# Optimization experiments

Hardware: AMD Instinct MI355X
Metric: run time of the kernel (lower is better)

The kernel has to match this reference:

```python
import jax, jax.numpy as jnp
import numpy as np

N = 100000
IN_CH = 128
OUT_CH = 40
K = 2
E = 3200000


def setup_inputs() -> dict:
    key = jax.random.key(0)
    k1, k2, k3, k4 = jax.random.split(key, 4)
    x = jax.random.normal(k1, (N, IN_CH), dtype=jnp.float32)
    edge_index = jax.random.randint(k2, (2, E), 0, N, dtype=jnp.int64)
    # Linear params (PyG Linear: glorot-style init approximated)
    scale = 1.0 / np.sqrt(IN_CH)
    W = jax.random.uniform(k3, (IN_CH, OUT_CH), dtype=jnp.float32, minval=-scale, maxval=scale)
    b = jax.random.uniform(k4, (OUT_CH,), dtype=jnp.float32, minval=-scale, maxval=scale)
    return {"x": x, "edge_index": edge_index, "W": W, "b": b}


def reference(x, edge_index, W, b):
    n = x.shape[0]
    row, col = edge_index[0], edge_index[1]  # source -> target
    # gcn_norm: add self loops, symmetric normalization
    loop = jnp.arange(n, dtype=row.dtype)
    row = jnp.concatenate([row, loop])
    col = jnp.concatenate([col, loop])
    ones = jnp.ones(row.shape[0], dtype=x.dtype)
    deg = jax.ops.segment_sum(ones, col, num_segments=n)  # in-degree incl. self-loop
    deg_inv_sqrt = jnp.where(deg > 0, jax.lax.rsqrt(deg), 0.0)
    norm = deg_inv_sqrt[row] * deg_inv_sqrt[col]  # [E+N]
    h = x
    for _ in range(K):
        # sparse SpMM: out[col] += norm * h[row]
        h = jax.ops.segment_sum(norm[:, None] * h[row], col, num_segments=n)
    logits = h @ W + b
    return jax.nn.log_softmax(logits, axis=-1)
```

## Files before the change

### kernel.cpp

```cpp
#include <hip/hip_runtime.h>
#include <hip/hip_fp16.h>
#include <math.h>

#define NN 100000
#define ICH 128
#define OCH 40
#define NE 3200000
#define BSH 8
#define BNODES 256
#define BMASK 255
#define NB 391
#define CAP 9216
#define TILE 4096
#define NBIN ((NE + TILE - 1) / TILE)
#define YSTRIDE 40
#define YU2 (YSTRIDE / 8)
#define XWBLK 1563

typedef __attribute__((ext_vector_type(2))) float floatx2;
typedef __attribute__((ext_vector_type(4))) float floatx4;
typedef __attribute__((ext_vector_type(8))) short bf16x8;

__device__ __forceinline__ unsigned int pk_bf16(float a, float b) {
    unsigned int r;
    asm("v_cvt_pk_bf16_f32 %0, %1, %2" : "=v"(r) : "v"(a), "v"(b));
    return r;
}

__device__ __forceinline__ void acc_fp8x8(const uint2 u, float* acc) {
    floatx2 p0 = __builtin_amdgcn_cvt_pk_f32_fp8((int)u.x, false);
    floatx2 p1 = __builtin_amdgcn_cvt_pk_f32_fp8((int)u.x, true);
    floatx2 p2 = __builtin_amdgcn_cvt_pk_f32_fp8((int)u.y, false);
    floatx2 p3 = __builtin_amdgcn_cvt_pk_f32_fp8((int)u.y, true);
    acc[0] += p0.x; acc[1] += p0.y; acc[2] += p1.x; acc[3] += p1.y;
    acc[4] += p2.x; acc[5] += p2.y; acc[6] += p3.x; acc[7] += p3.y;
}

__device__ __forceinline__ uint2 pack_fp8x8(const float* v) {
    int lo = 0, hi = 0;
    lo = __builtin_amdgcn_cvt_pk_fp8_f32(v[0], v[1], lo, false);
    lo = __builtin_amdgcn_cvt_pk_fp8_f32(v[2], v[3], lo, true);
    hi = __builtin_amdgcn_cvt_pk_fp8_f32(v[4], v[5], hi, false);
    hi = __builtin_amdgcn_cvt_pk_fp8_f32(v[6], v[7], hi, true);
    return make_uint2((unsigned int)lo, (unsigned int)hi);
}

__device__ __forceinline__ void row_gather(const int* __restrict__ csr, int kb, int ke, int q,
                                           const uint2* __restrict__ base, float* acc) {
    int k = kb;
    if (k + 8 <= ke) {
        int s[8];
        uint2 v[8];
#pragma unroll
        for (int j = 0; j < 8; ++j) s[j] = csr[k + j];
#pragma unroll
        for (int j = 0; j < 8; ++j) v[j] = base[(size_t)s[j] * YU2 + q];
        k += 8;
        for (; k + 8 <= ke; k += 8) {
            int s2[8];
            uint2 w[8];
#pragma unroll
            for (int j = 0; j < 8; ++j) s2[j] = csr[k + j];
#pragma unroll
            for (int j = 0; j < 8; ++j) w[j] = base[(size_t)s2[j] * YU2 + q];
#pragma unroll
            for (int j = 0; j < 8; ++j) acc_fp8x8(v[j], acc);
#pragma unroll
            for (int j = 0; j < 8; ++j) v[j] = w[j];
        }
#pragma unroll
        for (int j = 0; j < 8; ++j) acc_fp8x8(v[j], acc);
    }
    for (; k < ke; ++k) acc_fp8x8(base[(size_t)csr[k] * YU2 + q], acc);
}

__global__ __launch_bounds__(512) void k_bin(const int* __restrict__ ei, int* __restrict__ bcursor,
                                             unsigned int* __restrict__ packed,
                                             const float* __restrict__ W, unsigned int* __restrict__ wbf) {
    __shared__ unsigned int entries[TILE];
    __shared__ unsigned short bid[TILE];
    __shared__ int hist[512], base[512], gbase[512], cur[512];
    int t = threadIdx.x;
    int tile0 = blockIdx.x * TILE;
    int tcnt = min(TILE, NE - tile0);
    hist[t] = 0;
    __syncthreads();
    int src[8], dst[8];
#pragma unroll
    for (int i = 0; i < 8; ++i) {
        int l = t + i * 512;
        if (l < tcnt) {
            int e = tile0 + l;
            src[i] = ei[e];
            dst[i] = ei[NE + e];
            atomicAdd(&hist[dst[i] >> BSH], 1);
        } else dst[i] = -1;
    }
    __syncthreads();
    int own = hist[t];
    base[t] = own;
    __syncthreads();
    for (int off = 1; off < 512; off <<= 1) {
        int v = (t >= off) ? base[t - off] : 0;
        __syncthreads();
        base[t] += v;
        __syncthreads();
    }
    int excl = base[t] - own;
    __syncthreads();
    base[t] = excl;
    cur[t] = excl;
    if (t < NB && own > 0) gbase[t] = atomicAdd(&bcursor[t], own);
    __syncthreads();
#pragma unroll
    for (int i = 0; i < 8; ++i) {
        if (dst[i] >= 0) {
            int bb = dst[i] >> BSH;
            int pos = atomicAdd(&cur[bb], 1);
            entries[pos] = ((unsigned int)(dst[i] & BMASK) << 17) | (unsigned int)src[i];
            bid[pos] = (unsigned short)bb;
        }
    }
    __syncthreads();
    for (int l = t; l < tcnt; l += 512) {
        int bb = bid[l];
        packed[(size_t)bb * CAP + gbase[bb] + (l - base[bb])] = entries[l];
    }
    if (blockIdx.x == 0) {
        for (int e = t; e < 1536; e += 512) {
            int hs = e / 768;
            int rem = e - hs * 768;
            int ss = rem / 192;
            int rem2 = rem - ss * 192;
            int n = rem2 >> 6;
            int lane = rem2 & 63;
            int kbase = ss * 32 + (lane >> 4) * 8;
            int col = n * 16 + (lane & 15);
            unsigned int u4[4];
#pragma unroll
            for (int p = 0; p < 4; ++p) {
                float f0 = (col < OCH) ? W[(size_t)(kbase + 2 * p) * OCH + col] : 0.f;
                float f1 = (col < OCH) ? W[(size_t)(kbase + 2 * p + 1) * OCH + col] : 0.f;
                unsigned int h = pk_bf16(f0, f1);
                if (hs == 0) {
                    u4[p] = h;
                } else {
                    float l0 = f0 - __uint_as_float(h << 16);
                    float l1 = f1 - __uint_as_float(h & 0xFFFF0000u);
                    u4[p] = pk_bf16(l0, l1);
                }
            }
            ((uint4*)wbf)[e] = make_uint4(u4[0], u4[1], u4[2], u4[3]);
        }
    }
}

__global__ __launch_bounds__(512) void k_csr(const int* __restrict__ bcursor,
                                             const unsigned int* __restrict__ packed,
                                             int* __restrict__ rowptr, float* __restrict__ dis,
                                             int* __restrict__ csr) {
    __shared__ int hist[BNODES], cur[BNODES], ps[BNODES], sred[512];
    int b = blockIdx.x;
    int t = threadIdx.x;
    int part = 0;
    for (int j = t; j < b; j += 512) part += bcursor[j];
    sred[t] = part;
    if (t < BNODES) hist[t] = 0;
    __syncthreads();
    for (int off = 256; off > 0; off >>= 1) {
        if (t < off) sred[t] += sred[t + off];
        __syncthreads();
    }
    int cbase = sred[0];
    int cnt = bcursor[b];
    int node0 = b << BSH;
    int nn = min(BNODES, NN - node0);
    const unsigned int* pk = packed + (size_t)b * CAP;
    for (int l = t; l < cnt; l += 512) atomicAdd(&hist[pk[l] >> 17], 1);
    __syncthreads();
    if (t < BNODES) ps[t] = hist[t];
    __syncthreads();
    for (int off = 1; off < BNODES; off <<= 1) {
        int u = (t >= off && t < BNODES) ? ps[t - off] : 0;
        __syncthreads();
        if (t < BNODES) ps[t] += u;
        __syncthreads();
    }
    if (t < BNODES) {
        int excl = ps[t] - hist[t];
        cur[t] = excl;
        if (t < nn) {
            rowptr[node0 + t] = cbase + excl;
            dis[node0 + t] = rsqrtf((float)hist[t] + 1.0f);
        }
    }
    if (b == 0 && t == 0) rowptr[NN] = NE;
    __syncthreads();
    for (int l = t; l < cnt; l += 512) {
        unsigned int e = pk[l];
        int pos = atomicAdd(&cur[e >> 17], 1);
        csr[cbase + pos] = (int)(e & 0x1FFFF);
    }
}

__global__ __launch_bounds__(128) void k_xw(const float* __restrict__ x, const unsigned int* __restrict__ wbf,
                                            const float* __restrict__ dis, unsigned char* __restrict__ y0) {
    int t = threadIdx.x;
    int wid = t >> 6, lane = t & 63;
    const bf16x8* wf = (const bf16x8*)wbf;
    bf16x8 whi[4][3], wlo[4][3];
#pragma unroll
    for (int s = 0; s < 4; ++s)
#pragma unroll
        for (int n = 0; n < 3; ++n) {
            whi[s][n] = wf[(s * 3 + n) * 64 + lane];
            wlo[s][n] = wf[768 + (s * 3 + n) * 64 + lane];
        }
    int rbase = blockIdx.x * 64 + wid * 32;
#pragma unroll
    for (int tt = 0; tt < 2; ++tt) {
        int r0 = rbase + tt * 16;
        int rowa = r0 + (lane & 15);
        int rowc = min(rowa, NN - 1);
        int kb = (lane >> 4) * 8;
        const float4* xp = (const float4*)(x + (size_t)rowc * ICH + kb);
        float4 xa[4][2];
#pragma unroll
        for (int s = 0; s < 4; ++s) {
            xa[s][0] = xp[s * 8];
            xa[s][1] = xp[s * 8 + 1];
        }
        floatx4 acc[3] = {{0.f, 0.f, 0.f, 0.f}, {0.f, 0.f, 0.f, 0.f}, {0.f, 0.f, 0.f, 0.f}};
#pragma unroll
        for (int s = 0; s < 4; ++s) {
            float f[8] = {xa[s][0].x, xa[s][0].y, xa[s][0].z, xa[s][0].w,
                          xa[s][1].x, xa[s][1].y, xa[s][1].z, xa[s][1].w};
            union { unsigned int u[4]; bf16x8 v; } ah, al;
#pragma unroll
            for (int p = 0; p < 4; ++p) {
                unsigned int h = pk_bf16(f[2 * p], f[2 * p + 1]);
                ah.u[p] = h;
                float l0 = f[2 * p] - __uint_as_float(h << 16);
                float l1 = f[2 * p + 1] - __uint_as_float(h & 0xFFFF0000u);
                al.u[p] = pk_bf16(l0, l1);
            }
#pragma unroll
            for (int n = 0; n < 3; ++n) {
                acc[n] = __builtin_amdgcn_mfma_f32_16x16x32_bf16(ah.v, whi[s][n], acc[n], 0, 0, 0);
                acc[n] = __builtin_amdgcn_mfma_f32_16x16x32_bf16(al.v, whi[s][n], acc[n], 0, 0, 0);
                acc[n] = __builtin_amdgcn_mfma_f32_16x16x32_bf16(ah.v, wlo[s][n], acc[n], 0, 0, 0);
            }
        }
        int rc0 = r0 + (lane >> 4) * 4;
        float dd[4];
#pragma unroll
        for (int r = 0; r < 4; ++r) dd[r] = (rc0 + r < NN) ? dis[rc0 + r] : 0.f;
#pragma unroll
        for (int n = 0; n < 3; ++n) {
            int col = n * 16 + (lane & 15);
            if (col < OCH) {
#pragma unroll
                for (int r = 0; r < 4; ++r) {
                    int row = rc0 + r;
                    if (row < NN) {
                        float val = acc[n][r] * dd[r];
                        int p8 = __builtin_amdgcn_cvt_pk_fp8_f32(val, val, 0, false);
                        y0[(size_t)row * YSTRIDE + col] = (unsigned char)(p8 & 0xFF);
                    }
                }
            }
        }
    }
}

__global__ __launch_bounds__(256) void k_hop1(const int* __restrict__ rowptr, const int* __restrict__ csr,
                                              const float* __restrict__ dis, const unsigned char* __restrict__ y0,
                                              unsigned char* __restrict__ y1) {
    int g = blockIdx.x * 256 + threadIdx.x;
    if (g >= NN * 5) return;
    int i = g / 5, q = g - 5 * i;
    const uint2* base = (const uint2*)y0;
    float acc[8];
#pragma unroll
    for (int j = 0; j < 8; ++j) acc[j] = 0.f;
    acc_fp8x8(base[(size_t)i * YU2 + q], acc);
    row_gather(csr, rowptr[i], rowptr[i + 1], q, base, acc);
    float d = dis[i], d2 = d * d;
#pragma unroll
    for (int j = 0; j < 8; ++j) acc[j] *= d2;
    ((uint2*)y1)[(size_t)i * YU2 + q] = pack_fp8x8(acc);
}

__global__ __launch_bounds__(320) void k_hop2f(const int* __restrict__ rowptr, const int* __restrict__ csr,
                                               const float* __restrict__ dis, const unsigned char* __restrict__ y1,
                                               const float* __restrict__ b, float* __restrict__ out) {
    __shared__ float red[64][5];
    int tid = threadIdx.x;
    int lg = tid / 5;
    int q = tid - 5 * lg;
    int g = blockIdx.x * 64 + lg;
    bool active = (g < NN);
    float l[8];
    if (active) {
        const uint2* base = (const uint2*)y1;
        float acc[8];
#pragma unroll
        for (int j = 0; j < 8; ++j) acc[j] = 0.f;
        acc_fp8x8(base[(size_t)g * YU2 + q], acc);
        row_gather(csr, rowptr[g], rowptr[g + 1], q, base, acc);
        float d = dis[g];
#pragma unroll
        for (int j = 0; j < 8; ++j) l[j] = d * acc[j] + b[8 * q + j];
    } else {
#pragma unroll
        for (int j = 0; j < 8; ++j) l[j] = -1e30f;
    }
    float m8 = l[0];
#pragma unroll
    for (int j = 1; j < 8; ++j) m8 = fmaxf(m8, l[j]);
    red[lg][q] = m8;
    __syncthreads();
    float gm = red[lg][0];
#pragma unroll
    for (int j = 1; j < 5; ++j) gm = fmaxf(gm, red[lg][j]);
    __syncthreads();
    float s8 = 0.f;
#pragma unroll
    for (int j = 0; j < 8; ++j) s8 += __expf(l[j] - gm);
    red[lg][q] = s8;
    __syncthreads();
    float gs = red[lg][0];
#pragma unroll
    for (int j = 1; j < 5; ++j) gs += red[lg][j];
    float ls = __logf(gs) + gm;
    if (active) {
        floatx4* orow = (floatx4*)(out + (size_t)g * OCH + 8 * q);
        floatx4 o0 = {l[0] - ls, l[1] - ls, l[2] - ls, l[3] - ls};
        floatx4 o1 = {l[4] - ls, l[5] - ls, l[6] - ls, l[7] - ls};
        __builtin_nontemporal_store(o0, orow);
        __builtin_nontemporal_store(o1, orow + 1);
    }
}

extern "C" void kernel_launch(void* const* d_in, const int* in_sizes, int n_in,
                              void* d_out, int out_size, void* d_ws, size_t ws_size,
                              hipStream_t stream) {
    const float* x  = (const float*)d_in[0];
    const int*   ei = (const int*)d_in[1];
    const float* W  = (const float*)d_in[2];
    const float* b  = (const float*)d_in[3];
    float* out = (float*)d_out;

    char* ws = (char*)d_ws;
    int*           bcursor = (int*)(ws + 0);
    int*           rowptr  = (int*)(ws + 4096);
    float*         dis     = (float*)(ws + 409600);
    unsigned int*  wbf     = (unsigned int*)(ws + 811008);
    unsigned int*  packed  = (unsigned int*)(ws + 843776);
    unsigned char* y0      = (unsigned char*)(ws + 843776);
    unsigned char* y1      = (unsigned char*)(ws + 4849664);
    int*           csr     = (int*)(ws + 15261696);

    hipMemsetAsync(bcursor, 0, NB * sizeof(int), stream);
    k_bin<<<NBIN, 512, 0, stream>>>(ei, bcursor, packed, W, wbf);
    k_csr<<<NB, 512, 0, stream>>>(bcursor, packed, rowptr, dis, csr);
    k_xw<<<XWBLK, 128, 0, stream>>>(x, wbf, dis, y0);
    k_hop1<<<(NN * 5 + 255) / 256, 256, 0, stream>>>(rowptr, csr, dis, y0, y1);
    k_hop2f<<<(NN + 63) / 64, 320, 0, stream>>>(rowptr, csr, dis, y1, b, out);
}
```

Measured before the change: 238.2 us.

## Replace two-pass binned CSR build with global-atomic degree count and scatter

Replaces the tile-binning plus per-bucket CSR construction with a plain counting sort: global atomic degree histogram, block sums, per-block prefix scan into rowptr and a cursor array, then an atomic scatter of sources into csr. This drops the packed intermediate buffer and the shared-memory binning passes. In exchange it issues millions of global atomics on random addresses and writes csr in scattered order, which also makes the within-row edge order nondeterministic and loses locality in the scatter writes.

```diff
diff --git a/kernel.cpp b/kernel.cpp
--- a/kernel.cpp
+++ b/kernel.cpp
@@ -8,11 +8,7 @@
 #define NE 3200000
 #define BSH 8
 #define BNODES 256
-#define BMASK 255
 #define NB 391
-#define CAP 9216
-#define TILE 4096
-#define NBIN ((NE + TILE - 1) / TILE)
 #define YSTRIDE 40
 #define YU2 (YSTRIDE / 8)
 #define XWBLK 1563
@@ -74,60 +70,19 @@
     for (; k < ke; ++k) acc_fp8x8(base[(size_t)csr[k] * YU2 + q], acc);
 }
 
-__global__ __launch_bounds__(512) void k_bin(const int* __restrict__ ei, int* __restrict__ bcursor,
-                                             unsigned int* __restrict__ packed,
+__global__ __launch_bounds__(256) void k_deg(const int* __restrict__ ei, int* __restrict__ deg,
                                              const float* __restrict__ W, unsigned int* __restrict__ wbf) {
-    __shared__ unsigned int entries[TILE];
-    __shared__ unsigned short bid[TILE];
-    __shared__ int hist[512], base[512], gbase[512], cur[512];
-    int t = threadIdx.x;
-    int tile0 = blockIdx.x * TILE;
-    int tcnt = min(TILE, NE - tile0);
-    hist[t] = 0;
-    __syncthreads();
-    int src[8], dst[8];
-#pragma unroll
-    for (int i = 0; i < 8; ++i) {
-        int l = t + i * 512;
-        if (l < tcnt) {
-            int e = tile0 + l;
-            src[i] = ei[e];
-            dst[i] = ei[NE + e];
-            atomicAdd(&hist[dst[i] >> BSH], 1);
-        } else dst[i] = -1;
-    }
-    __syncthreads();
-    int own = hist[t];
-    base[t] = own;
-    __syncthreads();
-    for (int off = 1; off < 512; off <<= 1) {
-        int v = (t >= off) ? base[t - off] : 0;
-        __syncthreads();
-        base[t] += v;
-        __syncthreads();
-    }
-    int excl = base[t] - own;
-    __syncthreads();
-    base[t] = excl;
-    cur[t] = excl;
-    if (t < NB && own > 0) gbase[t] = atomicAdd(&bcursor[t], own);
-    __syncthreads();
-#pragma unroll
-    for (int i = 0; i < 8; ++i) {
-        if (dst[i] >= 0) {
-            int bb = dst[i] >> BSH;
-            int pos = atomicAdd(&cur[bb], 1);
-            entries[pos] = ((unsigned int)(dst[i] & BMASK) << 17) | (unsigned int)src[i];
-            bid[pos] = (unsigned short)bb;
-        }
-    }
-    __syncthreads();
-    for (int l = t; l < tcnt; l += 512) {
-        int bb = bid[l];
-        packed[(size_t)bb * CAP + gbase[bb] + (l - base[bb])] = entries[l];
+    int e0 = (blockIdx.x * 256 + threadIdx.x) * 4;
+    if (e0 < NE) {
+        int4 d = *(const int4*)(ei + NE + e0);
+        atomicAdd(&deg[d.x], 1);
+        atomicAdd(&deg[d.y], 1);
+        atomicAdd(&deg[d.z], 1);
+        atomicAdd(&deg[d.w], 1);
     }
     if (blockIdx.x == 0) {
-        for (int e = t; e < 1536; e += 512) {
+        int t = threadIdx.x;
+        for (int e = t; e < 1536; e += 256) {
             int hs = e / 768;
             int rem = e - hs * 768;
             int ss = rem / 192;
@@ -155,52 +110,66 @@
     }
 }
 
-__global__ __launch_bounds__(512) void k_csr(const int* __restrict__ bcursor,
-                                             const unsigned int* __restrict__ packed,
-                                             int* __restrict__ rowptr, float* __restrict__ dis,
-                                             int* __restrict__ csr) {
-    __shared__ int hist[BNODES], cur[BNODES], ps[BNODES], sred[512];
-    int b = blockIdx.x;
-    int t = threadIdx.x;
+__global__ __launch_bounds__(256) void k_bsum(const int* __restrict__ deg, int* __restrict__ bsum) {
+    __shared__ int s[256];
+    int b = blockIdx.x, t = threadIdx.x;
+    int node = (b << BSH) + t;
+    s[t] = (node < NN) ? deg[node] : 0;
+    __syncthreads();
+    for (int off = 128; off > 0; off >>= 1) {
+        if (t < off) s[t] += s[t + off];
+        __syncthreads();
+    }
+    if (t == 0) bsum[b] = s[0];
+}
+
+__global__ __launch_bounds__(256) void k_rowptr(const int* __restrict__ deg, const int* __restrict__ bsum,
+                                                int* __restrict__ rowptr, int* __restrict__ cur,
+                                                float* __restrict__ dis) {
+    __shared__ int sred[256], ps[BNODES];
+    int b = blockIdx.x, t = threadIdx.x;
     int part = 0;
-    for (int j = t; j < b; j += 512) part += bcursor[j];
+    for (int j = t; j < b; j += 256) part += bsum[j];
     sred[t] = part;
-    if (t < BNODES) hist[t] = 0;
-    __syncthreads();
-    for (int off = 256; off > 0; off >>= 1) {
+    __syncthreads();
+    for (int off = 128; off > 0; off >>= 1) {
         if (t < off) sred[t] += sred[t + off];
         __syncthreads();
     }
     int cbase = sred[0];
-    int cnt = bcursor[b];
-    int node0 = b << BSH;
-    int nn = min(BNODES, NN - node0);
-    const unsigned int* pk = packed + (size_t)b * CAP;
-    for (int l = t; l < cnt; l += 512) atomicAdd(&hist[pk[l] >> 17], 1);
-    __syncthreads();
-    if (t < BNODES) ps[t] = hist[t];
+    int node = (b << BSH) + t;
+    int d = (node < NN) ? deg[node] : 0;
+    ps[t] = d;
     __syncthreads();
     for (int off = 1; off < BNODES; off <<= 1) {
-        int u = (t >= off && t < BNODES) ? ps[t - off] : 0;
+        int u = (t >= off) ? ps[t - off] : 0;
         __syncthreads();
-        if (t < BNODES) ps[t] += u;
+        ps[t] += u;
         __syncthreads();
     }
-    if (t < BNODES) {
-        int excl = ps[t] - hist[t];
-        cur[t] = excl;
-        if (t < nn) {
-            rowptr[node0 + t] = cbase + excl;
-            dis[node0 + t] = rsqrtf((float)hist[t] + 1.0f);
-        }
+    if (node < NN) {
+        int excl = cbase + ps[t] - d;
+        rowptr[node] = excl;
+        cur[node] = excl;
+        dis[node] = rsqrtf((float)d + 1.0f);
     }
     if (b == 0 && t == 0) rowptr[NN] = NE;
-    __syncthreads();
-    for (int l = t; l < cnt; l += 512) {
-        unsigned int e = pk[l];
-        int pos = atomicAdd(&cur[e >> 17], 1);
-        csr[cbase + pos] = (int)(e & 0x1FFFF);
-    }
+}
+
+__global__ __launch_bounds__(256) void k_scat(const int* __restrict__ ei, int* __restrict__ cur,
+                                              int* __restrict__ csr) {
+    int e0 = (blockIdx.x * 256 + threadIdx.x) * 4;
+    if (e0 >= NE) return;
+    int4 s = *(const int4*)(ei + e0);
+    int4 d = *(const int4*)(ei + NE + e0);
+    int p0 = atomicAdd(&cur[d.x], 1);
+    int p1 = atomicAdd(&cur[d.y], 1);
+    int p2 = atomicAdd(&cur[d.z], 1);
+    int p3 = atomicAdd(&cur[d.w], 1);
+    csr[p0] = s.x;
+    csr[p1] = s.y;
+    csr[p2] = s.z;
+    csr[p3] = s.w;
 }
 
 __global__ __launch_bounds__(128) void k_xw(const float* __restrict__ x, const unsigned int* __restrict__ wbf,
@@ -352,18 +321,21 @@
     float* out = (float*)d_out;
 
     char* ws = (char*)d_ws;
-    int*           bcursor = (int*)(ws + 0);
-    int*           rowptr  = (int*)(ws + 4096);
-    float*         dis     = (float*)(ws + 409600);
-    unsigned int*  wbf     = (unsigned int*)(ws + 811008);
-    unsigned int*  packed  = (unsigned int*)(ws + 843776);
-    unsigned char* y0      = (unsigned char*)(ws + 843776);
-    unsigned char* y1      = (unsigned char*)(ws + 4849664);
-    int*           csr     = (int*)(ws + 15261696);
-
-    hipMemsetAsync(bcursor, 0, NB * sizeof(int), stream);
-    k_bin<<<NBIN, 512, 0, stream>>>(ei, bcursor, packed, W, wbf);
-    k_csr<<<NB, 512, 0, stream>>>(bcursor, packed, rowptr, dis, csr);
+    int*           rowptr = (int*)(ws + 0);
+    float*         dis    = (float*)(ws + 409600);
+    int*           deg    = (int*)(ws + 819200);
+    int*           cur    = (int*)(ws + 1228800);
+    int*           bsum   = (int*)(ws + 1630208);
+    unsigned int*  wbf    = (unsigned int*)(ws + 1638400);
+    unsigned char* y0     = (unsigned char*)(ws + 1703936);
+    unsigned char* y1     = (unsigned char*)(ws + 5709824);
+    int*           csr    = (int*)(ws + 9715712);
+
+    hipMemsetAsync(deg, 0, NN * sizeof(int), stream);
+    k_deg<<<(NE / 4 + 255) / 256, 256, 0, stream>>>(ei, deg, W, wbf);
+    k_bsum<<<NB, 256, 0, stream>>>(deg, bsum);
+    k_rowptr<<<NB, 256, 0, stream>>>(deg, bsum, rowptr, cur, dis);
+    k_scat<<<(NE / 4 + 255) / 256, 256, 0, stream>>>(ei, cur, csr);
     k_xw<<<XWBLK, 128, 0, stream>>>(x, wbf, dis, y0);
     k_hop1<<<(NN * 5 + 255) / 256, 256, 0, stream>>>(rowptr, csr, dis, y0, y1);
     k_hop2f<<<(NN + 63) / 64, 320, 0, stream>>>(rowptr, csr, dis, y1, b, out);
```

Result: slower. 597.1 us (+150.7%).

## Wave-align hop node groups, share CSR indices and reduce softmax via shuffles

Applied to the files above, without the earlier changes.

Both hop kernels now map each node's five lanes to a fixed group inside one wave, 12 nodes per wave and 48 per 256-thread block; the last 4 lanes of each wave sit idle. Within a group, four lanes each load two CSR neighbor indices as a uint2 and broadcast them with __shfl, replacing eight scalar index loads per lane. In the final hop, the log-softmax max and sum reductions move from shared memory with __syncthreads to in-wave shuffles. The aim is fewer redundant index loads and no block barriers, at the cost of about 6% idle lanes and uint2 CSR loads that may be only 4-byte aligned.

```diff
diff --git a/kernel.cpp b/kernel.cpp
--- a/kernel.cpp
+++ b/kernel.cpp
@@ -16,6 +16,8 @@
 #define YSTRIDE 40
 #define YU2 (YSTRIDE / 8)
 #define XWBLK 1563
+#define HOPNPB 48
+#define HOPGRID ((NN + HOPNPB - 1) / HOPNPB)
 
 typedef __attribute__((ext_vector_type(2))) float floatx2;
 typedef __attribute__((ext_vector_type(4))) float floatx4;
@@ -45,24 +47,30 @@
     return make_uint2((unsigned int)lo, (unsigned int)hi);
 }
 
-__device__ __forceinline__ void row_gather(const int* __restrict__ csr, int kb, int ke, int q,
-                                           const uint2* __restrict__ base, float* acc) {
+__device__ __forceinline__ void grp_csr8(const int* __restrict__ csr, int k, int q, int base, int* s) {
+    uint2 c = make_uint2(0u, 0u);
+    if (q < 4) c = *(const uint2*)(csr + k + 2 * q);
+#pragma unroll
+    for (int j = 0; j < 8; ++j)
+        s[j] = __shfl((j & 1) ? (int)c.y : (int)c.x, base + (j >> 1), 64);
+}
+
+__device__ __forceinline__ void row_gather(const int* __restrict__ csr, int kb, int ke, int q, int base,
+                                           const uint2* __restrict__ yb, float* acc) {
     int k = kb;
     if (k + 8 <= ke) {
         int s[8];
         uint2 v[8];
-#pragma unroll
-        for (int j = 0; j < 8; ++j) s[j] = csr[k + j];
-#pragma unroll
-        for (int j = 0; j < 8; ++j) v[j] = base[(size_t)s[j] * YU2 + q];
+        grp_csr8(csr, k, q, base, s);
+#pragma unroll
+        for (int j = 0; j < 8; ++j) v[j] = yb[(size_t)s[j] * YU2 + q];
         k += 8;
         for (; k + 8 <= ke; k += 8) {
             int s2[8];
             uint2 w[8];
-#pragma unroll
-            for (int j = 0; j < 8; ++j) s2[j] = csr[k + j];
-#pragma unroll
-            for (int j = 0; j < 8; ++j) w[j] = base[(size_t)s2[j] * YU2 + q];
+            grp_csr8(csr, k, q, base, s2);
+#pragma unroll
+            for (int j = 0; j < 8; ++j) w[j] = yb[(size_t)s2[j] * YU2 + q];
 #pragma unroll
             for (int j = 0; j < 8; ++j) acc_fp8x8(v[j], acc);
 #pragma unroll
@@ -71,7 +79,7 @@
 #pragma unroll
         for (int j = 0; j < 8; ++j) acc_fp8x8(v[j], acc);
     }
-    for (; k < ke; ++k) acc_fp8x8(base[(size_t)csr[k] * YU2 + q], acc);
+    for (; k < ke; ++k) acc_fp8x8(yb[(size_t)csr[k] * YU2 + q], acc);
 }
 
 __global__ __launch_bounds__(512) void k_bin(const int* __restrict__ ei, int* __restrict__ bcursor,
@@ -276,70 +284,61 @@
 __global__ __launch_bounds__(256) void k_hop1(const int* __restrict__ rowptr, const int* __restrict__ csr,
                                               const float* __restrict__ dis, const unsigned char* __restrict__ y0,
                                               unsigned char* __restrict__ y1) {
-    int g = blockIdx.x * 256 + threadIdx.x;
-    if (g >= NN * 5) return;
-    int i = g / 5, q = g - 5 * i;
-    const uint2* base = (const uint2*)y0;
+    int t = threadIdx.x;
+    int wave = t >> 6, lane = t & 63;
+    int grp = lane / 5, q = lane - 5 * grp;
+    int i = blockIdx.x * HOPNPB + wave * 12 + grp;
+    if (grp >= 12 || i >= NN) return;
+    int base = lane - q;
+    const uint2* yb = (const uint2*)y0;
     float acc[8];
 #pragma unroll
     for (int j = 0; j < 8; ++j) acc[j] = 0.f;
-    acc_fp8x8(base[(size_t)i * YU2 + q], acc);
-    row_gather(csr, rowptr[i], rowptr[i + 1], q, base, acc);
+    acc_fp8x8(yb[(size_t)i * YU2 + q], acc);
+    row_gather(csr, rowptr[i], rowptr[i + 1], q, base, yb, acc);
     float d = dis[i], d2 = d * d;
 #pragma unroll
     for (int j = 0; j < 8; ++j) acc[j] *= d2;
     ((uint2*)y1)[(size_t)i * YU2 + q] = pack_fp8x8(acc);
 }
 
-__global__ __launch_bounds__(320) void k_hop2f(const int* __restrict__ rowptr, const int* __restrict__ csr,
+__global__ __launch_bounds__(256) void k_hop2f(const int* __restrict__ rowptr, const int* __restrict__ csr,
                                                const float* __restrict__ dis, const unsigned char* __restrict__ y1,
                                                const float* __restrict__ b, float* __restrict__ out) {
-    __shared__ float red[64][5];
-    int tid = threadIdx.x;
-    int lg = tid / 5;
-    int q = tid - 5 * lg;
-    int g = blockIdx.x * 64 + lg;
-    bool active = (g < NN);
+    int t = threadIdx.x;
+    int wave = t >> 6, lane = t & 63;
+    int grp = lane / 5, q = lane - 5 * grp;
+    int g = blockIdx.x * HOPNPB + wave * 12 + grp;
+    if (grp >= 12 || g >= NN) return;
+    int base = lane - q;
+    const uint2* yb = (const uint2*)y1;
+    float acc[8];
+#pragma unroll
+    for (int j = 0; j < 8; ++j) acc[j] = 0.f;
+    acc_fp8x8(yb[(size_t)g * YU2 + q], acc);
+    row_gather(csr, rowptr[g], rowptr[g + 1], q, base, yb, acc);
+    float d = dis[g];
     float l[8];
-    if (active) {
-        const uint2* base = (const uint2*)y1;
-        float acc[8];
-#pragma unroll
-        for (int j = 0; j < 8; ++j) acc[j] = 0.f;
-        acc_fp8x8(base[(size_t)g * YU2 + q], acc);
-        row_gather(csr, rowptr[g], rowptr[g + 1], q, base, acc);
-        float d = dis[g];
-#pragma unroll
-        for (int j = 0; j < 8; ++j) l[j] = d * acc[j] + b[8 * q + j];
-    } else {
-#pragma unroll
-        for (int j = 0; j < 8; ++j) l[j] = -1e30f;
-    }
+#pragma unroll
+    for (int j = 0; j < 8; ++j) l[j] = d * acc[j] + b[8 * q + j];
     float m8 = l[0];
 #pragma unroll
     for (int j = 1; j < 8; ++j) m8 = fmaxf(m8, l[j]);
-    red[lg][q] = m8;
-    __syncthreads();
-    float gm = red[lg][0];
-#pragma unroll
-    for (int j = 1; j < 5; ++j) gm = fmaxf(gm, red[lg][j]);
-    __syncthreads();
+    float gm = m8;
+#pragma unroll
+    for (int j = 1; j < 5; ++j) gm = fmaxf(gm, __shfl(m8, base + j, 64));
     float s8 = 0.f;
 #pragma unroll
     for (int j = 0; j < 8; ++j) s8 += __expf(l[j] - gm);
-    red[lg][q] = s8;
-    __syncthreads();
-    float gs = red[lg][0];
-#pragma unroll
-    for (int j = 1; j < 5; ++j) gs += red[lg][j];
+    float gs = s8;
+#pragma unroll
+    for (int j = 1; j < 5; ++j) gs += __shfl(s8, base + j, 64);
     float ls = __logf(gs) + gm;
-    if (active) {
-        floatx4* orow = (floatx4*)(out + (size_t)g * OCH + 8 * q);
-        floatx4 o0 = {l[0] - ls, l[1] - ls, l[2] - ls, l[3] - ls};
-        floatx4 o1 = {l[4] - ls, l[5] - ls, l[6] - ls, l[7] - ls};
-        __builtin_nontemporal_store(o0, orow);
-        __builtin_nontemporal_store(o1, orow + 1);
-    }
+    floatx4* orow = (floatx4*)(out + (size_t)g * OCH + 8 * q);
+    floatx4 o0 = {l[0] - ls, l[1] - ls, l[2] - ls, l[3] - ls};
+    floatx4 o1 = {l[4] - ls, l[5] - ls, l[6] - ls, l[7] - ls};
+    __builtin_nontemporal_store(o0, orow);
+    __builtin_nontemporal_store(o1, orow + 1);
 }
 
 extern "C" void kernel_launch(void* const* d_in, const int* in_sizes, int n_in,
@@ -365,6 +364,6 @@
     k_bin<<<NBIN, 512, 0, stream>>>(ei, bcursor, packed, W, wbf);
     k_csr<<<NB, 512, 0, stream>>>(bcursor, packed, rowptr, dis, csr);
     k_xw<<<XWBLK, 128, 0, stream>>>(x, wbf, dis, y0);
-    k_hop1<<<(NN * 5 + 255) / 256, 256, 0, stream>>>(rowptr, csr, dis, y0, y1);
-    k_hop2f<<<(NN + 63) / 64, 320, 0, stream>>>(rowptr, csr, dis, y1, b, out);
-}
+    k_hop1<<<HOPGRID, 256, 0, stream>>>(rowptr, csr, dis, y0, y1);
+    k_hop2f<<<HOPGRID, 256, 0, stream>>>(rowptr, csr, dis, y1, b, out);
+}
```

After: 242.8 us. About the same (+1.9%).
